# Kernel optimization log

Hardware: AMD Instinct MI355X
Metric: run time of the kernel (lower is better)

## Reference

```python
import jax, jax.numpy as jnp
import numpy as np


def _grid_sample_bilinear_border(img, px, py):
    # img: [B,C,H,W]; px,py: [B,H,W] absolute pixel coords (align_corners=True)
    B, C, H, W = img.shape
    # border padding: clamp sample coords into valid range
    px = jnp.clip(px, 0.0, W - 1.0)
    py = jnp.clip(py, 0.0, H - 1.0)
    x0f = jnp.floor(px)
    y0f = jnp.floor(py)
    wx = px - x0f  # [B,H,W]
    wy = py - y0f
    x0 = jnp.clip(x0f.astype(jnp.int32), 0, W - 1)
    x1 = jnp.clip(x0 + 1, 0, W - 1)
    y0 = jnp.clip(y0f.astype(jnp.int32), 0, H - 1)
    y1 = jnp.clip(y0 + 1, 0, H - 1)

    flat = img.reshape(B, C, H * W)

    def gather(yi, xi):
        idx = (yi * W + xi).reshape(B, 1, H * W)
        return jnp.take_along_axis(flat, idx, axis=2).reshape(B, C, H, W)

    v00 = gather(y0, x0)
    v01 = gather(y0, x1)
    v10 = gather(y1, x0)
    v11 = gather(y1, x1)
    wx = wx[:, None]  # [B,1,H,W]
    wy = wy[:, None]
    top = v00 * (1.0 - wx) + v01 * wx
    bot = v10 * (1.0 - wx) + v11 * wx
    return top * (1.0 - wy) + bot * wy


def setup_inputs() -> dict:
    key = jax.random.key(0)
    k1, k2 = jax.random.split(key)
    B, C, H, W = 8, 64, 512, 512
    x = jax.random.normal(k1, (B, C, H, W), dtype=jnp.float32)
    flow = jax.random.normal(k2, (B, 2, H, W), dtype=jnp.float32)
    return {"x": x, "flow": flow}


def reference(x, flow):
    B, C, H, W = x.shape
    # Original builds a normalized grid then grid_sample unnormalizes it;
    # net effect: sample at absolute coords (gridX + u, gridY + v).
    gx = jnp.arange(W, dtype=x.dtype)[None, None, :]  # [1,1,W]
    gy = jnp.arange(H, dtype=x.dtype)[None, :, None]  # [1,H,1]
    px = gx + flow[:, 0]  # [B,H,W]
    py = gy + flow[:, 1]
    x_warp = _grid_sample_bilinear_border(x, px, py)
    return (x_warp, flow)
```

## Files before the change

kernel.cpp:

```cpp
#include <hip/hip_runtime.h>

#define BB 8
#define CC 64
#define HH 512
#define WW 512

__global__ __launch_bounds__(256) void align2d_warp_kernel(
    const float* __restrict__ x,
    const float* __restrict__ flow,
    float* __restrict__ out)
{
    const int tid = blockIdx.x * blockDim.x + threadIdx.x;
    const int w = tid & (WW - 1);
    const int h = (tid >> 9) & (HH - 1);
    const int b = tid >> 18;

    const int pix = h * WW + w;
    const float fx = flow[((size_t)b * 2 + 0) * (HH * WW) + pix];
    const float fy = flow[((size_t)b * 2 + 1) * (HH * WW) + pix];

    float px = fminf(fmaxf((float)w + fx, 0.0f), (float)(WW - 1));
    float py = fminf(fmaxf((float)h + fy, 0.0f), (float)(HH - 1));
    float x0f = floorf(px);
    float y0f = floorf(py);
    float wx = px - x0f;
    float wy = py - y0f;
    int x0 = (int)x0f;
    int y0 = (int)y0f;
    int x1 = min(x0 + 1, WW - 1);
    int y1 = min(y0 + 1, HH - 1);

    const int o00 = y0 * WW + x0;
    const int o01 = y0 * WW + x1;
    const int o10 = y1 * WW + x0;
    const int o11 = y1 * WW + x1;

    const float w00 = (1.0f - wx) * (1.0f - wy);
    const float w01 = wx * (1.0f - wy);
    const float w10 = (1.0f - wx) * wy;
    const float w11 = wx * wy;

    const float* xb = x   + (size_t)b * CC * HH * WW;
    float*       ob = out + (size_t)b * CC * HH * WW;

    #pragma unroll 4
    for (int c = 0; c < CC; ++c) {
        const float* p = xb + c * (HH * WW);
        float v = p[o00] * w00 + p[o01] * w01 + p[o10] * w10 + p[o11] * w11;
        ob[c * (HH * WW) + pix] = v;
    }
}

__global__ __launch_bounds__(256) void align2d_flowcopy_kernel(
    const float4* __restrict__ flow, float4* __restrict__ out)
{
    const int i = blockIdx.x * blockDim.x + threadIdx.x;
    out[i] = flow[i];
}

extern "C" void kernel_launch(void* const* d_in, const int* in_sizes, int n_in,
                              void* d_out, int out_size, void* d_ws, size_t ws_size,
                              hipStream_t stream) {
    const float* x    = (const float*)d_in[0];
    const float* flow = (const float*)d_in[1];
    float* out = (float*)d_out;

    const int npix = BB * HH * WW;
    align2d_warp_kernel<<<npix / 256, 256, 0, stream>>>(x, flow, out);

    const int nflow4 = (BB * 2 * HH * WW) / 4;
    float* out_flow = out + (size_t)BB * CC * HH * WW;
    align2d_flowcopy_kernel<<<nflow4 / 256, 256, 0, stream>>>(
        (const float4*)flow, (float4*)out_flow);
}
```

Measured before the change: 1.182 ms.

## Split channels into groups, remap blocks across XCDs, use nontemporal stores

Each thread now handles a 16-channel group instead of all 64 channels, which gives four times as many workgroups. Block IDs are remapped so that consecutive logical workgroups (neighbouring rows of the same batch and channel group) land on the same XCD. This is meant to improve L2 locality for the gathered neighbour reads and to raise memory-level parallelism. Output writes and the flow copy use nontemporal loads and stores to avoid polluting the cache. The trade-off is that flow values and bilinear weights are recomputed four times per pixel.

New measurement: 1.143 ms. 1.03x faster.

```diff
diff --git a/kernel.cpp b/kernel.cpp
--- a/kernel.cpp
+++ b/kernel.cpp
@@ -4,16 +4,29 @@
 #define CC 64
 #define HH 512
 #define WW 512
+#define CG 16
+#define NCG (CC / CG)
+#define NXCD 8
+
+typedef float f4 __attribute__((ext_vector_type(4)));
 
 __global__ __launch_bounds__(256) void align2d_warp_kernel(
     const float* __restrict__ x,
     const float* __restrict__ flow,
     float* __restrict__ out)
 {
-    const int tid = blockIdx.x * blockDim.x + threadIdx.x;
-    const int w = tid & (WW - 1);
-    const int h = (tid >> 9) & (HH - 1);
-    const int b = tid >> 18;
+    const int nwg = BB * NCG * HH * 2;
+    const int cpx = nwg / NXCD;
+    const int bid = blockIdx.x;
+    const int wg  = (bid % NXCD) * cpx + bid / NXCD;
+
+    const int b     = wg / (NCG * HH * 2);
+    int rem         = wg % (NCG * HH * 2);
+    const int cg    = rem / (HH * 2);
+    rem             = rem % (HH * 2);
+    const int h     = rem >> 1;
+    const int whalf = rem & 1;
+    const int w     = whalf * 256 + threadIdx.x;
 
     const int pix = h * WW + w;
     const float fx = flow[((size_t)b * 2 + 0) * (HH * WW) + pix];
@@ -40,22 +53,23 @@
     const float w10 = (1.0f - wx) * wy;
     const float w11 = wx * wy;
 
-    const float* xb = x   + (size_t)b * CC * HH * WW;
-    float*       ob = out + (size_t)b * CC * HH * WW;
+    const float* xb = x   + ((size_t)b * CC + (size_t)cg * CG) * (HH * WW);
+    float*       ob = out + ((size_t)b * CC + (size_t)cg * CG) * (HH * WW) + pix;
 
-    #pragma unroll 4
-    for (int c = 0; c < CC; ++c) {
-        const float* p = xb + c * (HH * WW);
+    #pragma unroll 8
+    for (int c = 0; c < CG; ++c) {
+        const float* p = xb + (size_t)c * (HH * WW);
         float v = p[o00] * w00 + p[o01] * w01 + p[o10] * w10 + p[o11] * w11;
-        ob[c * (HH * WW) + pix] = v;
+        __builtin_nontemporal_store(v, ob + (size_t)c * (HH * WW));
     }
 }
 
 __global__ __launch_bounds__(256) void align2d_flowcopy_kernel(
-    const float4* __restrict__ flow, float4* __restrict__ out)
+    const f4* __restrict__ flow, f4* __restrict__ out)
 {
     const int i = blockIdx.x * blockDim.x + threadIdx.x;
-    out[i] = flow[i];
+    f4 v = __builtin_nontemporal_load(flow + i);
+    __builtin_nontemporal_store(v, out + i);
 }
 
 extern "C" void kernel_launch(void* const* d_in, const int* in_sizes, int n_in,
@@ -65,11 +79,11 @@
     const float* flow = (const float*)d_in[1];
     float* out = (float*)d_out;
 
-    const int npix = BB * HH * WW;
-    align2d_warp_kernel<<<npix / 256, 256, 0, stream>>>(x, flow, out);
+    const int nwg = BB * NCG * HH * 2;
+    align2d_warp_kernel<<<nwg, 256, 0, stream>>>(x, flow, out);
 
     const int nflow4 = (BB * 2 * HH * WW) / 4;
     float* out_flow = out + (size_t)BB * CC * HH * WW;
     align2d_flowcopy_kernel<<<nflow4 / 256, 256, 0, stream>>>(
-        (const float4*)flow, (float4*)out_flow);
+        (const f4*)flow, (f4*)out_flow);
 }
```
